# Performance work log

Hardware: AMD Instinct MI355X
Metric: run time of the kernel (lower is better)

The kernel has to match this reference:

```python
import jax, jax.numpy as jnp
import numpy as np

L, B, D, H = 4096, 4, 1024, 16
HD = D // H
SCALAR = 700.0


def setup_inputs() -> dict:
    key = jax.random.key(0)
    ks = jax.random.split(key, 9)
    bound = np.sqrt(6.0 / (D + D)).astype(np.float32)  # xavier_uniform for square weights
    def xavier(k):
        return jax.random.uniform(k, (D, D), jnp.float32, -bound, bound)
    return {
        "input_tensor": jax.random.normal(ks[0], (L, B, D), jnp.float32),
        "num_heads": H,
        "Wq": xavier(ks[1]), "bq": jnp.zeros((D,), jnp.float32),
        "Wk": xavier(ks[2]), "bk": jnp.zeros((D,), jnp.float32),
        "Wv": xavier(ks[3]), "bv": jnp.zeros((D,), jnp.float32),
        "Wo": xavier(ks[4]), "bo": jnp.zeros((D,), jnp.float32),
        "scalar": jnp.asarray(SCALAR, jnp.float32),
    }


def reference(input_tensor, num_heads, Wq, bq, Wk, bk, Wv, bv, Wo, bo, scalar):
    l, b, d = input_tensor.shape
    h = num_heads
    hd = d // h
    scaling = hd ** -0.5
    X = jnp.transpose(input_tensor, (1, 0, 2))  # (b, l, d)
    q = (X @ Wq.T + bq) * scaling
    k = X @ Wk.T + bk
    v = X @ Wv.T + bv
    # split heads: (b, l, h*hd) -> (b, h, l, hd)
    q = q.reshape(b, l, h, hd).transpose(0, 2, 1, 3)
    k = k.reshape(b, l, h, hd).transpose(0, 2, 1, 3)
    v = v.reshape(b, l, h, hd).transpose(0, 2, 1, 3)
    # linear attention: (K^T V) then Q @ (...)  -> O(l * hd^2)
    kv = jnp.einsum('bhld,bhle->bhde', k, v)        # (b, h, hd, hd)
    out = jnp.einsum('bhld,bhde->bhle', q, kv) / scalar  # (b, h, l, hd)
    # faithful to einops '(b h) l d -> b l (d h)': feature layout is (hd, h)
    out = out.transpose(0, 2, 3, 1).reshape(b, l, d)  # (b, l, hd*h)
    out = out @ Wo.T + bo
    return jnp.transpose(out, (1, 0, 2))  # (l, b, d)
```

## Files before the change

### kernel.cpp

```cpp
#include <hip/hip_runtime.h>
#include <stdint.h>
#include <stddef.h>

typedef unsigned short ushort_t;
typedef __attribute__((ext_vector_type(8))) short short8;
typedef __attribute__((ext_vector_type(4))) float f32x4;
typedef __attribute__((ext_vector_type(4))) float float4v;

#define L_DIM 4096
#define B_DIM 4
#define D_DIM 1024
#define H_DIM 16
#define HD_DIM 64
#define M_DIM (L_DIM * B_DIM)

__device__ __forceinline__ float bf2f(ushort_t u) {
    union { unsigned int i; float f; } v; v.i = ((unsigned int)u) << 16; return v.f;
}
__device__ __forceinline__ ushort_t f2bf(float f) {
    union { float f; unsigned int i; } v; v.f = f;
    unsigned int r = v.i + 0x7FFFu + ((v.i >> 16) & 1u);
    return (ushort_t)(r >> 16);
}
__device__ __forceinline__ unsigned int pk2(float a, float b) {
    return (unsigned int)f2bf(a) | ((unsigned int)f2bf(b) << 16);
}
__device__ __forceinline__ void gload16(const ushort_t* g, ushort_t* l) {
    __builtin_amdgcn_global_load_lds(
        (const __attribute__((address_space(1))) unsigned int*)g,
        (__attribute__((address_space(3))) unsigned int*)l, 16, 0, 0);
}

__global__ void detect_kernel(const ushort_t* __restrict__ scal, int* __restrict__ flag)
{
    *flag = (scal[0] == 0) ? 1 : 0;
}

__global__ void convert_b_kernel(const void* bq, const void* bk, const void* bv,
                                 const void* bo, float* __restrict__ bias_f,
                                 const int* __restrict__ flag)
{
    int fl = *flag;
    int idx = blockIdx.x * 256 + threadIdx.x;
    int j = idx >> 10, i = idx & 1023;
    const void* p = (j == 0) ? bq : (j == 1) ? bk : (j == 2) ? bv : bo;
    bias_f[idx] = fl ? ((const float*)p)[i] : bf2f(((const ushort_t*)p)[i]);
}

__global__ void convert_w_kernel(const void* Wk, const void* Wv, const void* Wo,
                                 ushort_t* __restrict__ Wkc, ushort_t* __restrict__ Wvc,
                                 ushort_t* __restrict__ Wpc,
                                 const int* __restrict__ flag)
{
    int fl = *flag;
    int z = blockIdx.z;
    int idx = blockIdx.x * 256 + threadIdx.x;
    const void* src = (z == 0) ? Wk : (z == 1) ? Wv : Wo;
    ushort_t* dst   = (z == 0) ? Wkc : (z == 1) ? Wvc : Wpc;
    size_t sidx;
    if (z < 2) sidx = (size_t)idx;
    else {
        int n = idx >> 10, f = idx & 1023;
        int hh = f >> 6, e = f & 63;
        sidx = (size_t)n * D_DIM + e * H_DIM + hh;
    }
    dst[idx] = fl ? f2bf(((const float*)src)[sidx]) : ((const ushort_t*)src)[sidx];
}

__global__ void convert_x_kernel(const void* __restrict__ X, ushort_t* __restrict__ Xb,
                                 const int* __restrict__ flag)
{
    int fl = *flag;
    size_t i8 = ((size_t)blockIdx.x * 256 + threadIdx.x) * 8;
    if (fl) {
        const float4v* p = (const float4v*)((const float*)X + i8);
        float4v f0 = p[0], f1 = p[1];
        uint4 u;
        u.x = pk2(f0.x, f0.y); u.y = pk2(f0.z, f0.w);
        u.z = pk2(f1.x, f1.y); u.w = pk2(f1.z, f1.w);
        *(uint4*)(Xb + i8) = u;
    } else {
        *(uint4*)(Xb + i8) = *(const uint4*)((const ushort_t*)X + i8);
    }
}

__global__ __launch_bounds__(256) void proj_kernel(
    const ushort_t* __restrict__ A, int a_base0, int a_zstride, int astride,
    const ushort_t* __restrict__ W0, int w_z,
    const float* __restrict__ bias0, int b_z,
    void* __restrict__ out, int o_base0, int o_zstride, int ostride,
    const int* __restrict__ flag, int o_dyn)
{
    __shared__ ushort_t lA[128 * 32];
    __shared__ ushort_t lB[128 * 32];
    const int z    = blockIdx.z;
    const int a_base = a_base0 + z * a_zstride;
    const int o_base = o_base0 + z * o_zstride;
    const ushort_t* W = W0 + (size_t)z * w_z * (D_DIM * D_DIM);
    const float* bias = bias0 + z * b_z * D_DIM;
    const int ofl  = o_dyn & *flag;
    const int t    = threadIdx.x;
    const int m0   = blockIdx.x * 128;
    const int n0   = blockIdx.y * 128;
    const int w    = t >> 6;
    const int lane = t & 63;
    const int quad = lane >> 4;
    const int l16  = lane & 15;
    const int wm   = (w >> 1) * 64;
    const int wn   = (w & 1) * 64;

    const int c0 = t, c1 = t + 256;
    const int r0 = c0 >> 2, col0 = (c0 & 3) * 8;
    const int r1 = c1 >> 2, col1 = (c1 & 3) * 8;

    f32x4 acc[4][4];
#pragma unroll
    for (int i = 0; i < 4; i++)
#pragma unroll
        for (int j = 0; j < 4; j++) acc[i][j] = f32x4{0.f, 0.f, 0.f, 0.f};

    for (int k0 = 0; k0 < D_DIM; k0 += 32) {
        __syncthreads();
        gload16(A + (size_t)(a_base + (m0 + r0) * astride) * D_DIM + k0 + col0, &lA[c0 * 8]);
        gload16(A + (size_t)(a_base + (m0 + r1) * astride) * D_DIM + k0 + col1, &lA[c1 * 8]);
        gload16(W + (size_t)(n0 + r0) * D_DIM + k0 + col0, &lB[c0 * 8]);
        gload16(W + (size_t)(n0 + r1) * D_DIM + k0 + col1, &lB[c1 * 8]);
        __syncthreads();
        short8 af[4], bfr[4];
#pragma unroll
        for (int mt = 0; mt < 4; mt++)
            af[mt] = *(const short8*)&lA[(wm + mt * 16 + l16) * 32 + quad * 8];
#pragma unroll
        for (int nt = 0; nt < 4; nt++)
            bfr[nt] = *(const short8*)&lB[(wn + nt * 16 + l16) * 32 + quad * 8];
#pragma unroll
        for (int mt = 0; mt < 4; mt++)
#pragma unroll
            for (int nt = 0; nt < 4; nt++)
                acc[mt][nt] = __builtin_amdgcn_mfma_f32_16x16x32_bf16(
                    af[mt], bfr[nt], acc[mt][nt], 0, 0, 0);
    }

#pragma unroll
    for (int mt = 0; mt < 4; mt++) {
#pragma unroll
        for (int nt = 0; nt < 4; nt++) {
            int gn = n0 + wn + nt * 16 + l16;
            float bv = bias[gn];
#pragma unroll
            for (int i = 0; i < 4; i++) {
                int gm = m0 + wm + mt * 16 + quad * 4 + i;
                size_t oidx = (size_t)(o_base + gm * ostride) * D_DIM + gn;
                float val = acc[mt][nt][i] + bv;
                if (ofl) ((float*)out)[oidx] = val;
                else     ((ushort_t*)out)[oidx] = f2bf(val);
            }
        }
    }
}

__global__ __launch_bounds__(256) void kv_chunk_kernel(
    const ushort_t* __restrict__ kc, const ushort_t* __restrict__ vc,
    float* __restrict__ part, int lps)
{
    __shared__ ushort_t lkT[64 * 32];
    __shared__ ushort_t lvT[64 * 32];
    const int t    = threadIdx.x;
    const int s    = blockIdx.x;
    const int bh   = blockIdx.y;
    const int b    = bh >> 4, h = bh & 15;
    const int w    = t >> 6;
    const int lane = t & 63, quad = lane >> 4, l16 = lane & 15;

    f32x4 acc[4];
#pragma unroll
    for (int i = 0; i < 4; i++) acc[i] = f32x4{0.f, 0.f, 0.f, 0.f};

    const int niter = lps >> 5;
    for (int kt = 0; kt < niter; kt++) {
        int lcur = s * lps + kt * 32;
        __syncthreads();
#pragma unroll
        for (int i = 0; i < 4; i++) {
            int u  = t + 256 * i;
            int l  = u >> 5;
            int dp = u & 31;
            size_t goff = ((size_t)(lcur + l) * B_DIM + b) * D_DIM + h * HD_DIM + dp * 2;
            unsigned int kw = *(const unsigned int*)(kc + goff);
            unsigned int vw = *(const unsigned int*)(vc + goff);
            lkT[(2 * dp) * 32 + l]     = (ushort_t)kw;
            lkT[(2 * dp + 1) * 32 + l] = (ushort_t)(kw >> 16);
            lvT[(2 * dp) * 32 + l]     = (ushort_t)vw;
            lvT[(2 * dp + 1) * 32 + l] = (ushort_t)(vw >> 16);
        }
        __syncthreads();
        short8 af = *(const short8*)&lvT[(w * 16 + l16) * 32 + quad * 8];
#pragma unroll
        for (int dt = 0; dt < 4; dt++) {
            short8 bfr = *(const short8*)&lkT[(dt * 16 + l16) * 32 + quad * 8];
            acc[dt] = __builtin_amdgcn_mfma_f32_16x16x32_bf16(af, bfr, acc[dt], 0, 0, 0);
        }
    }
#pragma unroll
    for (int dt = 0; dt < 4; dt++) {
#pragma unroll
        for (int i = 0; i < 4; i++) {
            int e = w * 16 + quad * 4 + i;
            int d = dt * 16 + l16;
            part[(((size_t)s * 64 + bh) * 64 + e) * 64 + d] += acc[dt][i];
        }
    }
}

__global__ void kv_reduce_kernel(const float* __restrict__ part,
                                 ushort_t* __restrict__ kvT,
                                 const void* __restrict__ scal,
                                 const int* __restrict__ flag)
{
    int fl = *flag;
    float sc = fl ? *(const float*)scal : bf2f(((const ushort_t*)scal)[0]);
    float inv = 1.0f / sc;
    int idx = blockIdx.x * 256 + threadIdx.x;
    float sum = 0.0f;
#pragma unroll
    for (int s = 0; s < 8; s++) sum += part[((size_t)s << 18) + idx];
    kvT[idx] = f2bf(sum * inv);
}

__global__ __launch_bounds__(256) void wfuse_kernel(
    const void* __restrict__ Wq, const ushort_t* __restrict__ kvT,
    ushort_t* __restrict__ WfT, const int* __restrict__ flag)
{
    __shared__ ushort_t kvL[4096];
    const int fl = *flag;
    const int kt = blockIdx.x, h = blockIdx.y, b = blockIdx.z;
    const int t  = threadIdx.x;
    for (int i = t; i < 2048; i += 256)
        ((unsigned int*)kvL)[i] =
            ((const unsigned int*)(kvT + ((size_t)(b * 16 + h) << 12)))[i];
    __syncthreads();
    const int k  = kt * 128 + (t & 127);
    const int e0 = (t >> 7) * 32;
    float acc[32];
#pragma unroll
    for (int j = 0; j < 32; j++) acc[j] = 0.f;
    for (int d = 0; d < 64; d++) {
        size_t wi = (size_t)(h * 64 + d) * D_DIM + k;
        float wv = 0.125f * (fl ? ((const float*)Wq)[wi]
                                : bf2f(((const ushort_t*)Wq)[wi]));
#pragma unroll
        for (int j = 0; j < 32; j++)
            acc[j] += bf2f(kvL[(e0 + j) * 64 + d]) * wv;
    }
#pragma unroll
    for (int j = 0; j < 32; j++)
        WfT[((size_t)b * 1024 + k) * D_DIM + h * 64 + e0 + j] = f2bf(acc[j]);
}

__global__ void bias_fuse_kernel(const float* __restrict__ bq_f,
                                 const ushort_t* __restrict__ kvT,
                                 float* __restrict__ bfused)
{
    int idx = blockIdx.x * 256 + threadIdx.x;
    int b = idx >> 10, h = (idx >> 6) & 15, e = idx & 63;
    const ushort_t* kvp = kvT + ((size_t)(b * 16 + h) << 12) + e * 64;
    float s = 0.f;
#pragma unroll
    for (int d = 0; d < 64; d++) s += bf2f(kvp[d]) * bq_f[h * 64 + d];
    bfused[idx] = 0.125f * s;
}

__global__ void bias2_kernel(const ushort_t* __restrict__ Wpc,
                             const float* __restrict__ bfused,
                             const float* __restrict__ bo_f,
                             float* __restrict__ b2)
{
    int idx = blockIdx.x * 256 + threadIdx.x;
    int b = idx >> 10, n = idx & 1023;
    const ushort_t* wr = Wpc + (size_t)n * D_DIM;
    const float* bf = bfused + b * 1024;
    float s = 0.f;
    for (int f = 0; f < 1024; f++) s += bf2f(wr[f]) * bf[f];
    b2[idx] = s + bo_f[n];
}

extern "C" void kernel_launch(void* const* d_in, const int* in_sizes, int n_in,
                              void* d_out, int out_size, void* d_ws, size_t ws_size,
                              hipStream_t stream)
{
    const void* X    = d_in[0];
    const void* Wq   = d_in[2];
    const void* bq   = d_in[3];
    const void* Wk   = d_in[4];
    const void* bk   = d_in[5];
    const void* Wv   = d_in[6];
    const void* bv   = d_in[7];
    const void* Wo   = d_in[8];
    const void* bo   = d_in[9];
    const void* scal = d_in[10];

    char* ws = (char*)d_ws;
    int*      flag   = (int*)(ws + 0);
    float*    bias_f = (float*)(ws + 1024);
    float*    bfused = (float*)(ws + 32768);
    float*    b2     = (float*)(ws + 65536);
    float*    bias_z = (float*)(ws + 98304);
    ushort_t* Wkc    = (ushort_t*)(ws + 131072);
    ushort_t* Wvc    = (ushort_t*)(ws + 2228224);
    ushort_t* Wpc    = (ushort_t*)(ws + 4325376);
    ushort_t* kvT    = (ushort_t*)(ws + 6422528);
    float*    part   = (float*)(ws + 6946816);
    ushort_t* Xb     = (ushort_t*)(ws + 15335424);
    ushort_t* kvbuf  = (ushort_t*)(ws + 48889856);
    ushort_t* kc     = kvbuf;
    ushort_t* vc     = kvbuf + (size_t)8192 * D_DIM;
    ushort_t* WfT    = kvbuf;
    ushort_t* W2     = kvbuf + (size_t)4194304;

    detect_kernel<<<1, 1, 0, stream>>>((const ushort_t*)scal, flag);
    convert_b_kernel<<<16, 256, 0, stream>>>(bq, bk, bv, bo, bias_f, flag);
    convert_w_kernel<<<dim3(4096, 1, 3), 256, 0, stream>>>(Wk, Wv, Wo, Wkc, Wvc, Wpc, flag);
    convert_x_kernel<<<8192, 256, 0, stream>>>(X, Xb, flag);
    hipMemsetAsync(part, 0, 8388608, stream);
    hipMemsetAsync(bias_z, 0, 4096, stream);

    for (int c = 0; c < 2; c++) {
        proj_kernel<<<dim3(64, 8, 2), 256, 0, stream>>>(
            Xb, c * 8192, 0, 1,
            Wkc, 1,
            bias_f + 1024, 1,
            kvbuf, 0, 8192, 1,
            flag, 0);
        kv_chunk_kernel<<<dim3(8, 64), 256, 0, stream>>>(kc, vc, part, 256);
    }
    kv_reduce_kernel<<<1024, 256, 0, stream>>>(part, kvT, scal, flag);

    wfuse_kernel<<<dim3(8, 16, 4), 256, 0, stream>>>(Wq, kvT, WfT, flag);
    bias_fuse_kernel<<<16, 256, 0, stream>>>(bias_f, kvT, bfused);
    bias2_kernel<<<16, 256, 0, stream>>>(Wpc, bfused, bias_f + 3072, b2);

    proj_kernel<<<dim3(8, 8, 4), 256, 0, stream>>>(
        Wpc, 0, 0, 1,
        WfT, 1,
        bias_z, 0,
        W2, 0, 1024, 1,
        flag, 0);

    proj_kernel<<<dim3(32, 8, 4), 256, 0, stream>>>(
        Xb, 0, 1, 4,
        W2, 1,
        b2, 1,
        d_out, 0, 1, 4,
        flag, 1);
}
```

Baseline: 488.7 us.

## Rewrite projection GEMM as 256x256 double-buffered pipelined kernel with swizzled LDS

```diff
diff --git a/kernel.cpp b/kernel.cpp
--- a/kernel.cpp
+++ b/kernel.cpp
@@ -84,76 +84,132 @@
     }
 }
 
-__global__ __launch_bounds__(256) void proj_kernel(
+#define BARRIER() asm volatile("s_barrier" ::: "memory")
+#define VMWAIT(N) asm volatile("s_waitcnt vmcnt(" #N ")" ::: "memory")
+
+#define STAGE_A(q, kt, dbuf) {                                                 \
+    int kc_ = (kt) < 16 ? (kt) : 15;                                           \
+    int row_ = ((w & 4) << 5) + (q) * 32 + ((w & 3) << 3) + lrow8;             \
+    gload16(A + (size_t)(a_base + (m0 + row_) * astride) * D_DIM               \
+                + kc_ * 64 + kcol,                                             \
+            sA + (dbuf) * 16384 + row_ * 64 + lcol8); }
+
+#define STAGE_B(o, kt, dbuf) {                                                 \
+    int kc_ = (kt) < 16 ? (kt) : 15;                                           \
+    int nr_ = (o) * 64 + (w << 3) + lrow8;                                     \
+    gload16(W + (size_t)(n0 + nr_) * D_DIM + kc_ * 64 + kcol,                  \
+            sB + (dbuf) * 16384 + nr_ * 64 + lcol8); }
+
+#define PROJ_PHASE(S, STAGE0, STAGE1, WAITSTMT)                                \
+  {                                                                            \
+    short8 af[2][2];                                                           \
+    _Pragma("unroll")                                                          \
+    for (int j = 0; j < 2; ++j)                                                \
+      _Pragma("unroll")                                                        \
+      for (int ks = 0; ks < 2; ++ks)                                           \
+        af[j][ks] = *(const short8*)&lAc[(awbase + ((S) * 2 + j) * 16) * 64    \
+                                         + ((ks * 32 + q8) ^ swz)];            \
+    STAGE0; STAGE1;                                                            \
+    BARRIER();                                                                 \
+    __builtin_amdgcn_s_setprio(1);                                             \
+    _Pragma("unroll")                                                          \
+    for (int j = 0; j < 2; ++j)                                                \
+      _Pragma("unroll")                                                        \
+      for (int nt = 0; nt < 4; ++nt)                                           \
+        _Pragma("unroll")                                                      \
+        for (int ks = 0; ks < 2; ++ks)                                         \
+          acc[(S) * 2 + j][nt] = __builtin_amdgcn_mfma_f32_16x16x32_bf16(      \
+              af[j][ks], bf[nt][ks], acc[(S) * 2 + j][nt], 0, 0, 0);           \
+    __builtin_amdgcn_s_setprio(0);                                             \
+    WAITSTMT;                                                                  \
+    BARRIER();                                                                 \
+  }
+
+__global__ __launch_bounds__(512) void proj_kernel(
     const ushort_t* __restrict__ A, int a_base0, int a_zstride, int astride,
     const ushort_t* __restrict__ W0, int w_z,
     const float* __restrict__ bias0, int b_z,
     void* __restrict__ out, int o_base0, int o_zstride, int ostride,
     const int* __restrict__ flag, int o_dyn)
 {
-    __shared__ ushort_t lA[128 * 32];
-    __shared__ ushort_t lB[128 * 32];
-    const int z    = blockIdx.z;
+    extern __shared__ ushort_t smem[];
+    ushort_t* sA = smem;
+    ushort_t* sB = smem + 32768;
+
+    const int z      = blockIdx.z;
     const int a_base = a_base0 + z * a_zstride;
     const int o_base = o_base0 + z * o_zstride;
     const ushort_t* W = W0 + (size_t)z * w_z * (D_DIM * D_DIM);
     const float* bias = bias0 + z * b_z * D_DIM;
     const int ofl  = o_dyn & *flag;
     const int t    = threadIdx.x;
-    const int m0   = blockIdx.x * 128;
-    const int n0   = blockIdx.y * 128;
+    const int m0   = blockIdx.x * 256;
+    const int n0   = blockIdx.y * 256;
     const int w    = t >> 6;
     const int lane = t & 63;
     const int quad = lane >> 4;
     const int l16  = lane & 15;
-    const int wm   = (w >> 1) * 64;
-    const int wn   = (w & 1) * 64;
-
-    const int c0 = t, c1 = t + 256;
-    const int r0 = c0 >> 2, col0 = (c0 & 3) * 8;
-    const int r1 = c1 >> 2, col1 = (c1 & 3) * 8;
-
-    f32x4 acc[4][4];
-#pragma unroll
-    for (int i = 0; i < 4; i++)
+    const int wm   = w >> 2;
+    const int wn   = w & 3;
+
+    const int lrow8 = lane >> 3;
+    const int lcol8 = (lane & 7) * 8;
+    const int kcol  = (((lane & 7) ^ lrow8) << 3);
+
+    const int awbase = wm * 128 + l16;
+    const int bnbase = wn * 64 + l16;
+    const int q8     = quad * 8;
+    const int swz    = (l16 & 7) << 3;
+
+    f32x4 acc[8][4];
+#pragma unroll
+    for (int i = 0; i < 8; i++)
 #pragma unroll
         for (int j = 0; j < 4; j++) acc[i][j] = f32x4{0.f, 0.f, 0.f, 0.f};
 
-    for (int k0 = 0; k0 < D_DIM; k0 += 32) {
-        __syncthreads();
-        gload16(A + (size_t)(a_base + (m0 + r0) * astride) * D_DIM + k0 + col0, &lA[c0 * 8]);
-        gload16(A + (size_t)(a_base + (m0 + r1) * astride) * D_DIM + k0 + col1, &lA[c1 * 8]);
-        gload16(W + (size_t)(n0 + r0) * D_DIM + k0 + col0, &lB[c0 * 8]);
-        gload16(W + (size_t)(n0 + r1) * D_DIM + k0 + col1, &lB[c1 * 8]);
-        __syncthreads();
-        short8 af[4], bfr[4];
-#pragma unroll
-        for (int mt = 0; mt < 4; mt++)
-            af[mt] = *(const short8*)&lA[(wm + mt * 16 + l16) * 32 + quad * 8];
-#pragma unroll
-        for (int nt = 0; nt < 4; nt++)
-            bfr[nt] = *(const short8*)&lB[(wn + nt * 16 + l16) * 32 + quad * 8];
-#pragma unroll
-        for (int mt = 0; mt < 4; mt++)
-#pragma unroll
-            for (int nt = 0; nt < 4; nt++)
-                acc[mt][nt] = __builtin_amdgcn_mfma_f32_16x16x32_bf16(
-                    af[mt], bfr[nt], acc[mt][nt], 0, 0, 0);
-    }
-
-#pragma unroll
-    for (int mt = 0; mt < 4; mt++) {
-#pragma unroll
-        for (int nt = 0; nt < 4; nt++) {
-            int gn = n0 + wn + nt * 16 + l16;
-            float bv = bias[gn];
-#pragma unroll
-            for (int i = 0; i < 4; i++) {
-                int gm = m0 + wm + mt * 16 + quad * 4 + i;
-                size_t oidx = (size_t)(o_base + gm * ostride) * D_DIM + gn;
+    STAGE_B(0, 0, 0) STAGE_B(1, 0, 0) STAGE_B(2, 0, 0) STAGE_B(3, 0, 0)
+    STAGE_A(0, 0, 0) STAGE_A(1, 0, 0) STAGE_A(2, 0, 0) STAGE_A(3, 0, 0)
+    STAGE_B(0, 1, 1) STAGE_B(1, 1, 1)
+    VMWAIT(4);
+    BARRIER();
+
+    for (int c = 0; c < 16; ++c) {
+        const int buf = c & 1, nbuf = buf ^ 1;
+        const ushort_t* lAc = sA + buf * 16384;
+        const ushort_t* lBc = sB + buf * 16384;
+
+        short8 bf[4][2];
+#pragma unroll
+        for (int nt = 0; nt < 4; ++nt)
+#pragma unroll
+            for (int ks = 0; ks < 2; ++ks)
+                bf[nt][ks] = *(const short8*)&lBc[(bnbase + nt * 16) * 64
+                                                  + ((ks * 32 + q8) ^ swz)];
+
+        PROJ_PHASE(0, STAGE_B(2, c + 1, nbuf), STAGE_B(3, c + 1, nbuf), )
+        PROJ_PHASE(1, STAGE_A(0, c + 1, nbuf), STAGE_A(1, c + 1, nbuf), VMWAIT(6))
+        PROJ_PHASE(2, STAGE_A(2, c + 1, nbuf), STAGE_A(3, c + 1, nbuf), )
+        PROJ_PHASE(3, STAGE_B(0, c + 2, buf),  STAGE_B(1, c + 2, buf),  VMWAIT(4))
+    }
+
+#pragma unroll
+    for (int mt = 0; mt < 8; ++mt) {
+#pragma unroll
+        for (int nt = 0; nt < 4; ++nt) {
+            const int gn = n0 + wn * 64 + nt * 16 + l16;
+            const float bv = bias[gn];
+#pragma unroll
+            for (int i = 0; i < 4; ++i) {
+                const int gm = m0 + wm * 128 + mt * 16 + quad * 4 + i;
+                const size_t oidx = (size_t)(o_base + gm * ostride) * D_DIM + gn;
                 float val = acc[mt][nt][i] + bv;
-                if (ofl) ((float*)out)[oidx] = val;
-                else     ((ushort_t*)out)[oidx] = f2bf(val);
+                if (ofl) {
+                    ((float*)out)[oidx] = val;
+                } else {
+                    float v2 = __shfl_down(val, 1);
+                    if (!(l16 & 1))
+                        *(unsigned int*)((ushort_t*)out + oidx) = pk2(val, v2);
+                }
             }
         }
     }
@@ -298,6 +354,9 @@
     const void* Wo   = d_in[8];
     const void* bo   = d_in[9];
     const void* scal = d_in[10];
+
+    (void)hipFuncSetAttribute((const void*)proj_kernel,
+                              hipFuncAttributeMaxDynamicSharedMemorySize, 131072);
 
     char* ws = (char*)d_ws;
     int*      flag   = (int*)(ws + 0);
@@ -325,7 +384,7 @@
     hipMemsetAsync(bias_z, 0, 4096, stream);
 
     for (int c = 0; c < 2; c++) {
-        proj_kernel<<<dim3(64, 8, 2), 256, 0, stream>>>(
+        proj_kernel<<<dim3(32, 4, 2), 512, 131072, stream>>>(
             Xb, c * 8192, 0, 1,
             Wkc, 1,
             bias_f + 1024, 1,
@@ -339,14 +398,14 @@
     bias_fuse_kernel<<<16, 256, 0, stream>>>(bias_f, kvT, bfused);
     bias2_kernel<<<16, 256, 0, stream>>>(Wpc, bfused, bias_f + 3072, b2);
 
-    proj_kernel<<<dim3(8, 8, 4), 256, 0, stream>>>(
+    proj_kernel<<<dim3(4, 4, 4), 512, 131072, stream>>>(
         Wpc, 0, 0, 1,
         WfT, 1,
         bias_z, 0,
         W2, 0, 1024, 1,
         flag, 0);
 
-    proj_kernel<<<dim3(32, 8, 4), 256, 0, stream>>>(
+    proj_kernel<<<dim3(16, 4, 4), 512, 131072, stream>>>(
         Xb, 0, 1, 4,
         W2, 1,
         b2, 1,
```

After: 459.7 us. 5.9% less time.
